# Kernel optimization log

Measured on AMD Instinct MI355X. Metric: run time of the kernel, lower is better.

Reference implementation:

```python
import jax, jax.numpy as jnp
import numpy as np

K = 5  # kernel_size


def conv1d(x, w, b, pad):
    # x: (B,C,T), w: (O,I,k), NCH/OIH/NCH
    out = jax.lax.conv_general_dilated(
        x, w, window_strides=(1,), padding=[(pad, pad)],
        dimension_numbers=('NCH', 'OIH', 'NCH'))
    return out + b[None, :, None]


def setup_inputs() -> dict:
    key = jax.random.key(0)
    ks = jax.random.split(key, 10)
    B, C, T = 16, 256, 4096
    s = 0.05  # keep conv pre-activations in a sane range
    return {
        'x': jax.random.normal(ks[0], (B, C, T), jnp.float32),
        'offset_w': jax.random.normal(ks[1], (2 * K, C, 3), jnp.float32) * s,
        'offset_b': jax.random.normal(ks[2], (2 * K,), jnp.float32) * s,
        'mod_w': jax.random.normal(ks[3], (K, C, 3), jnp.float32) * s,
        'mod_b': jax.random.normal(ks[4], (K,), jnp.float32) * s,
        'weight': jax.random.normal(ks[5], (C, C, K), jnp.float32),
        'rp1_w': jax.random.normal(ks[6], (C // 2, C, 3), jnp.float32) * s,
        'rp1_b': jax.random.normal(ks[7], (C // 2,), jnp.float32) * s,
        'rp2_w': jax.random.normal(ks[8], (1, C // 2, 1), jnp.float32) * s,
        'rp2_b': jax.random.normal(ks[9], (1,), jnp.float32) * s,
    }


def reference(x, offset_w, offset_b, mod_w, mod_b, weight, rp1_w, rp1_b, rp2_w, rp2_b):
    B, C, T = x.shape
    offset = conv1d(x, offset_w, offset_b, 1)                 # (B,2K,T)
    modulator = jax.nn.sigmoid(conv1d(x, mod_w, mod_b, 1))    # (B,K,T)

    # offset.view(B,2,K,T).permute(0,3,1,2) -> (B,T,2,K); only [:, :, 0, :] used
    off = offset.reshape(B, 2, K, T).transpose(0, 3, 1, 2)[:, :, 0, :]  # (B,T,K)
    modp = modulator.transpose(0, 2, 1)                       # (B,T,K)

    base = jnp.arange(T, dtype=x.dtype)[None, :, None]        # (1,T,1)
    kpos = (jnp.arange(K, dtype=x.dtype) - K // 2)[None, None, :]  # (1,1,K)
    pos = jnp.clip(base + kpos + off, 0.0, T - 1)             # (B,T,K)

    pf = jnp.floor(pos)
    pc = jnp.ceil(pos)
    wf = pc - pos                                             # floor weight
    wc = pos - pf                                             # ceil weight
    pfi = jnp.clip(pf.astype(jnp.int32), 0, T - 1)
    pci = jnp.clip(pc.astype(jnp.int32), 0, T - 1)

    # gather along T: x (B,C,1,T), idx (B,1,T,K) -> (B,C,T,K)
    sf = jnp.take_along_axis(x[:, :, None, :], pfi[:, None, :, :], axis=3)
    sc = jnp.take_along_axis(x[:, :, None, :], pci[:, None, :, :], axis=3)
    sampled = sf * wf[:, None, :, :] + sc * wc[:, None, :, :]  # (B,C,T,K)

    diag_w = weight[jnp.arange(C), jnp.arange(C), :]           # (C,K)
    deformed = jnp.einsum('bctk,ck,btk->bct', sampled, diag_w, modp)

    h = jax.nn.relu(conv1d(deformed, rp1_w, rp1_b, 1))         # (B,C//2,T)
    recovery = conv1d(h, rp2_w, rp2_b, 0)[:, 0, :]             # (B,T)
    return deformed, recovery
```

## Files before the change

kernel.cpp:

```cpp
#include <hip/hip_runtime.h>
#include <hip/hip_bf16.h>
#include <math.h>

#define B_  16
#define C_  256
#define T_  4096
#define K_  5

typedef __attribute__((ext_vector_type(4))) float floatx4;
typedef __attribute__((ext_vector_type(8))) short short8;



__global__ __launch_bounds__(256) void k0_setup(
    const float* __restrict__ ow, const float* __restrict__ mw,
    const float* __restrict__ wt, const float* __restrict__ r1w,
    float* __restrict__ wk1, float* __restrict__ diagw,
    __hip_bfloat16* __restrict__ w_r)
{
    int idx = blockIdx.x * 256 + threadIdx.x;
    if (idx < 98304) {
        int o = idx / 768; int rem = idx - o * 768; int c = rem / 3; int d = rem - c * 3;
        w_r[(size_t)(d * 128 + o) * 256 + c] = __float2bfloat16(r1w[idx]);
    }
    if (idx < 7680) {
        int d = idx / 2560; int rem = idx - d * 2560; int c = rem / 10; int f = rem - c * 10;
        wk1[idx] = (f < 5) ? ow[(f * C_ + c) * 3 + d] : mw[((f - 5) * C_ + c) * 3 + d];
    }
    if (idx < 1280) {
        int c = idx / 5; int k = idx - c * 5;
        diagw[idx] = wt[((size_t)c * C_ + c) * K_ + k];
    }
}

#define LOADG(BUF, GG) do { \
    _Pragma("unroll") \
    for (int i_ = 0; i_ < 16; ++i_) \
        BUF[i_] = xp[(size_t)((GG) * 16 + i_) * T_]; \
} while (0)

#define PROCG(BUF, GG) do { \
    _Pragma("unroll") \
    for (int i_ = 0; i_ < 16; ++i_) { \
        const float v_ = inb ? BUF[i_] : 0.f; \
        const float* wr_ = wbase + ((GG) * 16 + i_) * 10; \
        { \
            _Pragma("clang fp contract(off)") \
            float q0 = wr_[0] * v_; so0 = so0 + q0; \
            float q1 = wr_[1] * v_; so1 = so1 + q1; \
            float q2 = wr_[2] * v_; so2 = so2 + q2; \
            float q3 = wr_[3] * v_; so3 = so3 + q3; \
            float q4 = wr_[4] * v_; so4 = so4 + q4; \
        } \
        am0 = fmaf(wr_[5], v_, am0); \
        am1 = fmaf(wr_[6], v_, am1); \
        am2 = fmaf(wr_[7], v_, am2); \
        am3 = fmaf(wr_[8], v_, am3); \
        am4 = fmaf(wr_[9], v_, am4); \
    } \
} while (0)

__global__ __launch_bounds__(256) void k12_fused(
    const float* __restrict__ x,
    const float* __restrict__ wk1,
    const float* __restrict__ ob, const float* __restrict__ mb,
    const float* __restrict__ diagw,
    float* __restrict__ dout)
{
    __shared__ float staps[3][K_][64];
    __shared__ float smod[3][K_][64];
    __shared__ int   spf[K_][64];
    __shared__ int   spc[K_][64];
    __shared__ float swa[K_][64];
    __shared__ float swb[K_][64];
    const int t0  = blockIdx.x * 64;
    const int b   = blockIdx.y;
    const int tid = threadIdx.x;
    const int tl  = tid & 63;
    const int wv  = tid >> 6;
    const int t   = t0 + tl;

    if (wv < 3) {
        const int wvu = __builtin_amdgcn_readfirstlane(wv);
        const int dd  = wvu - 1;
        const bool inb = ((unsigned)(t + dd) < (unsigned)T_);
        const float* xp = x + (size_t)b * C_ * T_ + t + (inb ? dd : 0);
        const float* wbase = wk1 + wvu * 2560;
        float so0=0.f, so1=0.f, so2=0.f, so3=0.f, so4=0.f;
        float am0=0.f, am1=0.f, am2=0.f, am3=0.f, am4=0.f;
        float pA[16], pB[16], pC[16];
        LOADG(pA, 0); LOADG(pB, 1); LOADG(pC, 2);
#pragma unroll
        for (int g = 0; g < 16; g += 3) {
            PROCG(pA, g);
            if (g + 3 < 16) LOADG(pA, g + 3);
            if (g + 1 < 16) { PROCG(pB, g + 1); if (g + 4 < 16) LOADG(pB, g + 4); }
            if (g + 2 < 16) { PROCG(pC, g + 2); if (g + 5 < 16) LOADG(pC, g + 5); }
        }
        staps[wvu][0][tl] = so0; staps[wvu][1][tl] = so1; staps[wvu][2][tl] = so2;
        staps[wvu][3][tl] = so3; staps[wvu][4][tl] = so4;
        smod[wvu][0][tl]  = am0; smod[wvu][1][tl]  = am1; smod[wvu][2][tl]  = am2;
        smod[wvu][3][tl]  = am3; smod[wvu][4][tl]  = am4;
    }
    __syncthreads();

    if (tid < 64) {
#pragma clang fp contract(off)
#pragma unroll
        for (int k = 0; k < K_; ++k) {
            float offv = ((staps[0][k][tl] + staps[1][k][tl]) + staps[2][k][tl]) + ob[k];
            float modv = ((smod[0][k][tl] + smod[1][k][tl]) + smod[2][k][tl]) + mb[k];
            float sig  = 1.f / (1.f + expf(-modv));
            float pos  = (float)(t + k - 2) + offv;
            pos = fminf(fmaxf(pos, 0.f), 4095.f);
            float pf = floorf(pos), pc = ceilf(pos);
            spf[k][tl] = (int)pf;
            spc[k][tl] = (int)pc;
            swa[k][tl] = (pc - pos) * sig;
            swb[k][tl] = (pos - pf) * sig;
        }
    }
    __syncthreads();

    const int cgU = __builtin_amdgcn_readfirstlane(wv);
    int   pfk[K_], pck[K_];
    float ak[K_], bk[K_];
#pragma unroll
    for (int k = 0; k < K_; ++k) {
        pfk[k] = spf[k][tl]; pck[k] = spc[k][tl];
        ak[k]  = swa[k][tl]; bk[k]  = swb[k][tl];
    }
    const float* xr  = x    + (size_t)(b * C_ + cgU * 64) * T_;
    float*       dp  = dout + (size_t)(b * C_ + cgU * 64) * T_ + t;
    const float* dwp = diagw + cgU * 320;
    float vfA[K_], vcA[K_], vfB[K_], vcB[K_];
#pragma unroll
    for (int k = 0; k < K_; ++k) {
        vfA[k] = xr[pfk[k]];              vcA[k] = xr[pck[k]];
        vfB[k] = xr[T_ + pfk[k]];         vcB[k] = xr[T_ + pck[k]];
    }
    for (int j = 0; j < 64; j += 2) {
        float nfA[K_], ncA[K_], nfB[K_], ncB[K_];
        if (j < 62) {
            const float* xa  = xr + (size_t)(j + 2) * T_;
            const float* xb2 = xr + (size_t)(j + 3) * T_;
#pragma unroll
            for (int k = 0; k < K_; ++k) {
                nfA[k] = xa[pfk[k]];  ncA[k] = xa[pck[k]];
                nfB[k] = xb2[pfk[k]]; ncB[k] = xb2[pck[k]];
            }
        }
        float a0 = 0.f, a1 = 0.f;
#pragma unroll
        for (int k = 0; k < K_; ++k) {
            a0 += dwp[j * 5 + k]       * (vfA[k] * ak[k] + vcA[k] * bk[k]);
            a1 += dwp[(j + 1) * 5 + k] * (vfB[k] * ak[k] + vcB[k] * bk[k]);
        }
        dp[(size_t)j * T_]       = a0;
        dp[(size_t)(j + 1) * T_] = a1;
        if (j < 62) {
#pragma unroll
            for (int k = 0; k < K_; ++k) {
                vfA[k] = nfA[k]; vcA[k] = ncA[k];
                vfB[k] = nfB[k]; vcB[k] = ncB[k];
            }
        }
    }
}

__global__ __launch_bounds__(256) void k3_rp(
    const float* __restrict__ ddef,
    const __hip_bfloat16* __restrict__ w_r,
    const float* __restrict__ rp1b, const float* __restrict__ rp2w,
    const float* __restrict__ rp2b,
    float* __restrict__ rec)
{
    __shared__ __align__(16) short lw[3 * 128 * 40];
    __shared__ __align__(16) short ld[66 * 40];
    const int t0 = blockIdx.x * 64;
    const int b  = blockIdx.y;
    const int tid  = threadIdx.x;
    const int lane = tid & 63;
    const int w    = tid >> 6;
    const int qd   = lane >> 4;
    const int ln   = lane & 15;

    floatx4 acc[8];
#pragma unroll
    for (int m = 0; m < 8; ++m) acc[m] = (floatx4){0.f, 0.f, 0.f, 0.f};

    for (int ch = 0; ch < 8; ++ch) {
        int c0 = ch * 32;
        __syncthreads();
        for (int f = tid; f < 1536; f += 256) {
            int c8 = (f & 3) * 8;
            int o  = (f >> 2) & 127;
            int d  = f >> 9;
            *(int4*)&lw[(d * 128 + o) * 40 + c8] =
                *(const int4*)((const short*)w_r + (size_t)(d * 128 + o) * 256 + c0 + c8);
        }
        for (int f = tid; f < 32 * 66; f += 256) {
            int c = f / 66;
            int j = f - c * 66;
            int g = t0 - 1 + j;
            float v = (g >= 0 && g < T_) ? ddef[(size_t)(b * C_ + c0 + c) * T_ + g] : 0.f;
            __hip_bfloat16 h = __float2bfloat16(v);
            ld[j * 40 + c] = *(short*)&h;
        }
        __syncthreads();
#pragma unroll
        for (int d = 0; d < 3; ++d) {
            short8 bf = *(const short8*)&ld[(w * 16 + ln + d) * 40 + qd * 8];
#pragma unroll
            for (int m = 0; m < 8; ++m) {
                short8 af = *(const short8*)&lw[(d * 128 + m * 16 + ln) * 40 + qd * 8];
                acc[m] = __builtin_amdgcn_mfma_f32_16x16x32_bf16(af, bf, acc[m], 0, 0, 0);
            }
        }
    }

    float rv = 0.f;
#pragma unroll
    for (int m = 0; m < 8; ++m)
#pragma unroll
        for (int r = 0; r < 4; ++r) {
            int o = m * 16 + qd * 4 + r;
            float h = acc[m][r] + rp1b[o];
            h = h > 0.f ? h : 0.f;
            rv += rp2w[o] * h;
        }
    rv += __shfl_xor(rv, 16);
    rv += __shfl_xor(rv, 32);
    if (qd == 0)
        rec[b * T_ + t0 + w * 16 + ln] = rv + rp2b[0];
}

extern "C" void kernel_launch(void* const* d_in, const int* in_sizes, int n_in,
                              void* d_out, int out_size, void* d_ws, size_t ws_size,
                              hipStream_t stream) {
    const float* x   = (const float*)d_in[0];
    const float* ow  = (const float*)d_in[1];
    const float* ob  = (const float*)d_in[2];
    const float* mw  = (const float*)d_in[3];
    const float* mb  = (const float*)d_in[4];
    const float* wt  = (const float*)d_in[5];
    const float* r1w = (const float*)d_in[6];
    const float* r1b = (const float*)d_in[7];
    const float* r2w = (const float*)d_in[8];
    const float* r2b = (const float*)d_in[9];

    char* ws = (char*)d_ws;
    float*          wk1   = (float*)(ws + 0);
    float*          diagw = (float*)(ws + 30720);
    __hip_bfloat16* w_r   = (__hip_bfloat16*)(ws + 35840);

    float* dout = (float*)d_out;
    float* rec  = (float*)d_out + (size_t)B_ * C_ * T_;

    k0_setup<<<384, 256, 0, stream>>>(ow, mw, wt, r1w, wk1, diagw, w_r);
    k12_fused<<<dim3(T_ / 64, B_), 256, 0, stream>>>(x, wk1, ob, mb, diagw, dout);
    k3_rp<<<dim3(T_ / 64, B_), 256, 0, stream>>>(dout, w_r, r1b, r2w, r2b, rec);
}
```

Baseline: 282.6 us.

## Stage x window in LDS for deformable gather and prefetch rp conv tiles

In the fused offset/deform kernel, the otherwise idle fourth wave stages a 256-channel by 80-sample window of x into shared memory while the other waves compute offsets. Each deformable gather then reads from LDS, falling back to global loads only for lanes whose sampled positions leave the window. In the recovery-path MFMA kernel, the next channel chunk of weights and activations is loaded into registers while the current chunk is computed, overlapping global loads with MFMA work. The cost is about 80 KB of LDS per block, which lowers occupancy, plus more registers for the prefetch buffers.

```diff
diff --git a/kernel.cpp b/kernel.cpp
--- a/kernel.cpp
+++ b/kernel.cpp
@@ -67,6 +67,7 @@
     const float* __restrict__ diagw,
     float* __restrict__ dout)
 {
+    __shared__ __align__(16) float sx[256 * 80 + 4];
     __shared__ float staps[3][K_][64];
     __shared__ float smod[3][K_][64];
     __shared__ int   spf[K_][64];
@@ -101,6 +102,27 @@
         staps[wvu][3][tl] = so3; staps[wvu][4][tl] = so4;
         smod[wvu][0][tl]  = am0; smod[wvu][1][tl]  = am1; smod[wvu][2][tl]  = am2;
         smod[wvu][3][tl]  = am3; smod[wvu][4][tl]  = am4;
+    } else {
+        const float* xb = x + (size_t)b * C_ * T_;
+        if (t0 >= 8 && t0 + 72 <= T_) {
+            const float* src = xb + (t0 - 8);
+            int c = tl / 20, q = tl - (tl / 20) * 20;
+            for (int it = 0; it < 80; ++it) {
+                *(float4*)&sx[c * 80 + q * 4] =
+                    *(const float4*)(src + (size_t)c * T_ + q * 4);
+                q += 4; c += 3;
+                if (q >= 20) { q -= 20; c += 1; }
+            }
+        } else {
+            int c = 0, col = tl;
+            for (int it = 0; it < 320; ++it) {
+                int g = t0 - 8 + col;
+                sx[c * 80 + col] = ((unsigned)g < (unsigned)T_)
+                                 ? xb[(size_t)c * T_ + g] : 0.f;
+                col += 64;
+                if (col >= 80) { col -= 80; c += 1; }
+            }
+        }
     }
     __syncthreads();
 
@@ -123,48 +145,45 @@
     __syncthreads();
 
     const int cgU = __builtin_amdgcn_readfirstlane(wv);
-    int   pfk[K_], pck[K_];
+    int   pfk[K_], pck[K_], ibase[K_];
     float ak[K_], bk[K_];
+    bool  ow_[K_];
+    bool  outl = false;
 #pragma unroll
     for (int k = 0; k < K_; ++k) {
         pfk[k] = spf[k][tl]; pck[k] = spc[k][tl];
         ak[k]  = swa[k][tl]; bk[k]  = swb[k][tl];
-    }
-    const float* xr  = x    + (size_t)(b * C_ + cgU * 64) * T_;
-    float*       dp  = dout + (size_t)(b * C_ + cgU * 64) * T_ + t;
-    const float* dwp = diagw + cgU * 320;
-    float vfA[K_], vcA[K_], vfB[K_], vcB[K_];
-#pragma unroll
-    for (int k = 0; k < K_; ++k) {
-        vfA[k] = xr[pfk[k]];              vcA[k] = xr[pck[k]];
-        vfB[k] = xr[T_ + pfk[k]];         vcB[k] = xr[T_ + pck[k]];
-    }
-    for (int j = 0; j < 64; j += 2) {
-        float nfA[K_], ncA[K_], nfB[K_], ncB[K_];
-        if (j < 62) {
-            const float* xa  = xr + (size_t)(j + 2) * T_;
-            const float* xb2 = xr + (size_t)(j + 3) * T_;
-#pragma unroll
-            for (int k = 0; k < K_; ++k) {
-                nfA[k] = xa[pfk[k]];  ncA[k] = xa[pck[k]];
-                nfB[k] = xb2[pfk[k]]; ncB[k] = xb2[pck[k]];
-            }
-        }
-        float a0 = 0.f, a1 = 0.f;
+        int xf = pfk[k] - (t0 - 8);
+        int xc = pck[k] - (t0 - 8);
+        ow_[k] = ((unsigned)xf >= 80u) | ((unsigned)xc >= 80u);
+        outl  |= ow_[k];
+        ibase[k] = ow_[k] ? 0 : xf;
+    }
+    const bool anyout = __any(outl);
+    const float* lx   = &sx[cgU * 64 * 80];
+    const float* dwp  = diagw + cgU * 320;
+    float*       dp   = dout + (size_t)(b * C_ + cgU * 64) * T_ + t;
+    const float* xrow0 = x + (size_t)(b * C_ + cgU * 64) * T_;
+
+#pragma unroll 4
+    for (int j = 0; j < 64; ++j) {
+        float vf[K_], vc[K_];
 #pragma unroll
         for (int k = 0; k < K_; ++k) {
-            a0 += dwp[j * 5 + k]       * (vfA[k] * ak[k] + vcA[k] * bk[k]);
-            a1 += dwp[(j + 1) * 5 + k] * (vfB[k] * ak[k] + vcB[k] * bk[k]);
-        }
-        dp[(size_t)j * T_]       = a0;
-        dp[(size_t)(j + 1) * T_] = a1;
-        if (j < 62) {
-#pragma unroll
-            for (int k = 0; k < K_; ++k) {
-                vfA[k] = nfA[k]; vcA[k] = ncA[k];
-                vfB[k] = nfB[k]; vcB[k] = ncB[k];
-            }
-        }
+            vf[k] = lx[j * 80 + ibase[k]];
+            vc[k] = lx[j * 80 + ibase[k] + 1];
+        }
+        if (anyout) {
+            const float* xrow = xrow0 + (size_t)j * T_;
+#pragma unroll
+            for (int k = 0; k < K_; ++k)
+                if (ow_[k]) { vf[k] = xrow[pfk[k]]; vc[k] = xrow[pck[k]]; }
+        }
+        float a0 = 0.f;
+#pragma unroll
+        for (int k = 0; k < K_; ++k)
+            a0 += dwp[j * 5 + k] * (vf[k] * ak[k] + vc[k] * bk[k]);
+        dp[(size_t)j * T_] = a0;
     }
 }
 
@@ -184,30 +203,62 @@
     const int w    = tid >> 6;
     const int qd   = lane >> 4;
     const int ln   = lane & 15;
+    const short* wsrc = (const short*)w_r;
 
     floatx4 acc[8];
 #pragma unroll
     for (int m = 0; m < 8; ++m) acc[m] = (floatx4){0.f, 0.f, 0.f, 0.f};
 
+    int wo[6], wd[6], wc8[6];
+#pragma unroll
+    for (int i = 0; i < 6; ++i) {
+        int f = tid + i * 256;
+        wc8[i] = (f & 3) * 8;
+        wo[i]  = (f >> 2) & 127;
+        wd[i]  = f >> 9;
+    }
+    int sc[9], sj[9];
+#pragma unroll
+    for (int i = 0; i < 9; ++i) {
+        int f = tid + i * 256;
+        sc[i] = f / 66;
+        sj[i] = f - sc[i] * 66;
+    }
+
+    int4  wreg[6];
+    float dreg[9];
+#define K3_LOADW(CH) do { \
+    _Pragma("unroll") \
+    for (int i_ = 0; i_ < 6; ++i_) \
+        wreg[i_] = *(const int4*)(wsrc + (size_t)(wd[i_] * 128 + wo[i_]) * 256 \
+                                  + (CH) * 32 + wc8[i_]); \
+} while (0)
+#define K3_LOADD(CH) do { \
+    _Pragma("unroll") \
+    for (int i_ = 0; i_ < 9; ++i_) { \
+        if (tid + i_ * 256 < 2112) { \
+            int g_ = t0 - 1 + sj[i_]; \
+            dreg[i_] = ((unsigned)g_ < (unsigned)T_) \
+                     ? ddef[(size_t)(b * C_ + (CH) * 32 + sc[i_]) * T_ + g_] : 0.f; \
+        } \
+    } \
+} while (0)
+
+    K3_LOADW(0); K3_LOADD(0);
+
     for (int ch = 0; ch < 8; ++ch) {
-        int c0 = ch * 32;
+#pragma unroll
+        for (int i = 0; i < 6; ++i)
+            *(int4*)&lw[(wd[i] * 128 + wo[i]) * 40 + wc8[i]] = wreg[i];
+#pragma unroll
+        for (int i = 0; i < 9; ++i) {
+            if (tid + i * 256 < 2112) {
+                __hip_bfloat16 h = __float2bfloat16(dreg[i]);
+                ld[sj[i] * 40 + sc[i]] = *(short*)&h;
+            }
+        }
         __syncthreads();
-        for (int f = tid; f < 1536; f += 256) {
-            int c8 = (f & 3) * 8;
-            int o  = (f >> 2) & 127;
-            int d  = f >> 9;
-            *(int4*)&lw[(d * 128 + o) * 40 + c8] =
-                *(const int4*)((const short*)w_r + (size_t)(d * 128 + o) * 256 + c0 + c8);
-        }
-        for (int f = tid; f < 32 * 66; f += 256) {
-            int c = f / 66;
-            int j = f - c * 66;
-            int g = t0 - 1 + j;
-            float v = (g >= 0 && g < T_) ? ddef[(size_t)(b * C_ + c0 + c) * T_ + g] : 0.f;
-            __hip_bfloat16 h = __float2bfloat16(v);
-            ld[j * 40 + c] = *(short*)&h;
-        }
-        __syncthreads();
+        if (ch < 7) { K3_LOADW(ch + 1); K3_LOADD(ch + 1); }
 #pragma unroll
         for (int d = 0; d < 3; ++d) {
             short8 bf = *(const short8*)&ld[(w * 16 + ln + d) * 40 + qd * 8];
@@ -217,6 +268,7 @@
                 acc[m] = __builtin_amdgcn_mfma_f32_16x16x32_bf16(af, bf, acc[m], 0, 0, 0);
             }
         }
+        __syncthreads();
     }
 
     float rv = 0.f;
```

Result: slower. 436.1 us (+54.3%).

## Split fused offset/gather kernel into offset kernel and channel-parallel gather kernel

Applied to the files above, without the earlier changes.

The fused offset+gather kernel is split in two. The first kernel computes the offset/modulator convolutions and writes floor indices and the modulated interpolation weights to workspace. The second kernel spreads the gather over 4 channel groups per time tile, stages a haloed x tile in LDS and reads samples from it, falling back to global memory for out-of-window positions. This raises grid parallelism and coalesces the gather, at the cost of an extra launch, a workspace round trip and a fallback path when the workspace is too small.

```diff
diff --git a/kernel.cpp b/kernel.cpp
--- a/kernel.cpp
+++ b/kernel.cpp
@@ -11,6 +11,7 @@
 typedef __attribute__((ext_vector_type(8))) short short8;
 
 
+#define WS_NEED 3509248
 
 __global__ __launch_bounds__(256) void k0_setup(
     const float* __restrict__ ow, const float* __restrict__ mw,
@@ -60,7 +61,153 @@
     } \
 } while (0)
 
-__global__ __launch_bounds__(256) void k12_fused(
+#define PHASE_A_BODY(STAPS, SMOD) do { \
+    const int wvu = __builtin_amdgcn_readfirstlane(wv); \
+    const int dd  = wvu - 1; \
+    const bool inb = ((unsigned)(t + dd) < (unsigned)T_); \
+    const float* xp = x + (size_t)b * C_ * T_ + t + (inb ? dd : 0); \
+    const float* wbase = wk1 + wvu * 2560; \
+    float so0=0.f, so1=0.f, so2=0.f, so3=0.f, so4=0.f; \
+    float am0=0.f, am1=0.f, am2=0.f, am3=0.f, am4=0.f; \
+    float pA[16], pB[16], pC[16]; \
+    LOADG(pA, 0); LOADG(pB, 1); LOADG(pC, 2); \
+    _Pragma("unroll") \
+    for (int g = 0; g < 16; g += 3) { \
+        PROCG(pA, g); \
+        if (g + 3 < 16) LOADG(pA, g + 3); \
+        if (g + 1 < 16) { PROCG(pB, g + 1); if (g + 4 < 16) LOADG(pB, g + 4); } \
+        if (g + 2 < 16) { PROCG(pC, g + 2); if (g + 5 < 16) LOADG(pC, g + 5); } \
+    } \
+    STAPS[wvu][0][tl] = so0; STAPS[wvu][1][tl] = so1; STAPS[wvu][2][tl] = so2; \
+    STAPS[wvu][3][tl] = so3; STAPS[wvu][4][tl] = so4; \
+    SMOD[wvu][0][tl]  = am0; SMOD[wvu][1][tl]  = am1; SMOD[wvu][2][tl]  = am2; \
+    SMOD[wvu][3][tl]  = am3; SMOD[wvu][4][tl]  = am4; \
+} while (0)
+
+__global__ __launch_bounds__(192) void k1_off(
+    const float* __restrict__ x,
+    const float* __restrict__ wk1,
+    const float* __restrict__ ob, const float* __restrict__ mb,
+    short* __restrict__ wpf, float* __restrict__ wwa, float* __restrict__ wwb)
+{
+    __shared__ float staps[3][K_][64];
+    __shared__ float smod[3][K_][64];
+    const int t0  = blockIdx.x * 64;
+    const int b   = blockIdx.y;
+    const int tid = threadIdx.x;
+    const int tl  = tid & 63;
+    const int wv  = tid >> 6;
+    const int t   = t0 + tl;
+
+    PHASE_A_BODY(staps, smod);
+    __syncthreads();
+
+    if (tid < 64) {
+#pragma clang fp contract(off)
+#pragma unroll
+        for (int k = 0; k < K_; ++k) {
+            float offv = ((staps[0][k][tl] + staps[1][k][tl]) + staps[2][k][tl]) + ob[k];
+            float modv = ((smod[0][k][tl] + smod[1][k][tl]) + smod[2][k][tl]) + mb[k];
+            float sig  = 1.f / (1.f + expf(-modv));
+            float pos  = (float)(t + k - 2) + offv;
+            pos = fminf(fmaxf(pos, 0.f), 4095.f);
+            float pf = floorf(pos), pc = ceilf(pos);
+            wpf[(size_t)(b * 5 + k) * T_ + t] = (short)(int)pf;
+            wwa[(size_t)(b * 5 + k) * T_ + t] = (pc - pos) * sig;
+            wwb[(size_t)(b * 5 + k) * T_ + t] = (pos - pf) * sig;
+        }
+    }
+}
+
+__global__ __launch_bounds__(256) void k2_gather(
+    const float* __restrict__ x,
+    const float* __restrict__ diagw,
+    const short* __restrict__ wpf, const float* __restrict__ wwa,
+    const float* __restrict__ wwb,
+    float* __restrict__ dout)
+{
+    __shared__ __align__(16) float sx[64 * 80 + 4];
+    const int t0 = blockIdx.x * 64;
+    const int cg = blockIdx.y;
+    const int b  = blockIdx.z;
+    const int c0 = cg * 64;
+    const int tid = threadIdx.x;
+    const int tl  = tid & 63;
+    const int wv  = __builtin_amdgcn_readfirstlane(tid >> 6);
+    const int t   = t0 + tl;
+
+    const float* xb = x + (size_t)(b * C_ + c0) * T_;
+
+    if (t0 >= 8 && t0 + 72 <= T_) {
+#pragma unroll
+        for (int i = 0; i < 5; ++i) {
+            int f = tid + i * 256;
+            int r = f / 20, q = f - r * 20;
+            *(float4*)&sx[r * 80 + q * 4] =
+                *(const float4*)(xb + (size_t)r * T_ + (t0 - 8) + q * 4);
+        }
+    } else {
+#pragma unroll
+        for (int i = 0; i < 5; ++i) {
+            int f = tid + i * 256;
+            int r = f / 20, q = f - r * 20;
+#pragma unroll
+            for (int e = 0; e < 4; ++e) {
+                int g = t0 - 8 + q * 4 + e;
+                sx[r * 80 + q * 4 + e] = ((unsigned)g < (unsigned)T_)
+                                       ? xb[(size_t)r * T_ + g] : 0.f;
+            }
+        }
+    }
+
+    int pfg[K_], ib[K_];
+    float ak[K_], bk[K_];
+    bool ow_[K_];
+    bool o = false;
+#pragma unroll
+    for (int k = 0; k < K_; ++k) {
+        pfg[k] = (int)wpf[(size_t)(b * 5 + k) * T_ + t];
+        ak[k]  = wwa[(size_t)(b * 5 + k) * T_ + t];
+        bk[k]  = wwb[(size_t)(b * 5 + k) * T_ + t];
+        ib[k]  = pfg[k] - (t0 - 8);
+        ow_[k] = ((unsigned)ib[k] > 78u);
+        o |= ow_[k];
+        if (ow_[k]) ib[k] = 0;
+    }
+    const bool anyout = __any(o);
+    __syncthreads();
+
+    float* dp = dout + (size_t)(b * C_ + c0) * T_ + t;
+#pragma unroll 4
+    for (int j = 0; j < 16; ++j) {
+        const int cl = wv * 16 + j;
+        const float* lx = &sx[cl * 80];
+        float vf[K_], vc[K_];
+#pragma unroll
+        for (int k = 0; k < K_; ++k) {
+            vf[k] = lx[ib[k]];
+            vc[k] = lx[ib[k] + 1];
+        }
+        if (anyout) {
+            const float* xr = xb + (size_t)cl * T_;
+#pragma unroll
+            for (int k = 0; k < K_; ++k)
+                if (ow_[k]) {
+                    int pi = pfg[k];
+                    int ci = pi + 1 > 4095 ? 4095 : pi + 1;
+                    vf[k] = xr[pi]; vc[k] = xr[ci];
+                }
+        }
+        const float* dw = diagw + (c0 + cl) * 5;
+        float acc = 0.f;
+#pragma unroll
+        for (int k = 0; k < K_; ++k)
+            acc += dw[k] * (vf[k] * ak[k] + vc[k] * bk[k]);
+        dp[(size_t)cl * T_] = acc;
+    }
+}
+
+__global__ __launch_bounds__(256) void k12_fallback(
     const float* __restrict__ x,
     const float* __restrict__ wk1,
     const float* __restrict__ ob, const float* __restrict__ mb,
@@ -81,26 +228,7 @@
     const int t   = t0 + tl;
 
     if (wv < 3) {
-        const int wvu = __builtin_amdgcn_readfirstlane(wv);
-        const int dd  = wvu - 1;
-        const bool inb = ((unsigned)(t + dd) < (unsigned)T_);
-        const float* xp = x + (size_t)b * C_ * T_ + t + (inb ? dd : 0);
-        const float* wbase = wk1 + wvu * 2560;
-        float so0=0.f, so1=0.f, so2=0.f, so3=0.f, so4=0.f;
-        float am0=0.f, am1=0.f, am2=0.f, am3=0.f, am4=0.f;
-        float pA[16], pB[16], pC[16];
-        LOADG(pA, 0); LOADG(pB, 1); LOADG(pC, 2);
-#pragma unroll
-        for (int g = 0; g < 16; g += 3) {
-            PROCG(pA, g);
-            if (g + 3 < 16) LOADG(pA, g + 3);
-            if (g + 1 < 16) { PROCG(pB, g + 1); if (g + 4 < 16) LOADG(pB, g + 4); }
-            if (g + 2 < 16) { PROCG(pC, g + 2); if (g + 5 < 16) LOADG(pC, g + 5); }
-        }
-        staps[wvu][0][tl] = so0; staps[wvu][1][tl] = so1; staps[wvu][2][tl] = so2;
-        staps[wvu][3][tl] = so3; staps[wvu][4][tl] = so4;
-        smod[wvu][0][tl]  = am0; smod[wvu][1][tl]  = am1; smod[wvu][2][tl]  = am2;
-        smod[wvu][3][tl]  = am3; smod[wvu][4][tl]  = am4;
+        PHASE_A_BODY(staps, smod);
     }
     __syncthreads();
 
@@ -253,11 +381,19 @@
     float*          wk1   = (float*)(ws + 0);
     float*          diagw = (float*)(ws + 30720);
     __hip_bfloat16* w_r   = (__hip_bfloat16*)(ws + 35840);
+    short*          wpf   = (short*)(ws + 232448);
+    float*          wwa   = (float*)(ws + 887808);
+    float*          wwb   = (float*)(ws + 2198528);
 
     float* dout = (float*)d_out;
     float* rec  = (float*)d_out + (size_t)B_ * C_ * T_;
 
     k0_setup<<<384, 256, 0, stream>>>(ow, mw, wt, r1w, wk1, diagw, w_r);
-    k12_fused<<<dim3(T_ / 64, B_), 256, 0, stream>>>(x, wk1, ob, mb, diagw, dout);
+    if (ws_size >= (size_t)WS_NEED) {
+        k1_off<<<dim3(T_ / 64, B_), 192, 0, stream>>>(x, wk1, ob, mb, wpf, wwa, wwb);
+        k2_gather<<<dim3(T_ / 64, 4, B_), 256, 0, stream>>>(x, diagw, wpf, wwa, wwb, dout);
+    } else {
+        k12_fallback<<<dim3(T_ / 64, B_), 256, 0, stream>>>(x, wk1, ob, mb, diagw, dout);
+    }
     k3_rp<<<dim3(T_ / 64, B_), 256, 0, stream>>>(dout, w_r, r1b, r2w, r2b, rec);
 }
```

Result: faster. 252.1 us (-10.8%).
